# Optimization experiments

Hardware: AMD Instinct MI355X
Metric: run time of the kernel (lower is better)

Reference implementation:

```python
import jax, jax.numpy as jnp
import numpy as np

N_E = 1024
E_DIM = 512
LEGACY_CLUSTER = 0.2
LEGACY_ENERGY = 0.2


def setup_inputs() -> dict:
    key = jax.random.key(0)
    k1, k2 = jax.random.split(key)
    B, T = 64, 512
    key_soft = jax.random.normal(k1, (B, T, E_DIM), dtype=jnp.float32)
    zero_ts_mask = jnp.zeros((B,), dtype=bool)
    # nn.Embedding(1+n_e, e_dim) initialized uniform(-1/n_e, 1/n_e)
    emb_weight = jax.random.uniform(k2, (N_E + 1, E_DIM), dtype=jnp.float32,
                                    minval=-1.0 / N_E, maxval=1.0 / N_E)
    return {"key_soft": key_soft, "zero_ts_mask": zero_ts_mask, "emb_weight": emb_weight}


def _compute_indices(d3, zero_ts_mask, n_e):
    # d3: [B, T, n_e+1] squared distances (treated as constants: torch.no_grad)
    ind0 = jnp.clip(jnp.argmin(d3[:, 0, :], axis=1), 0, n_e - 1)
    ind0 = jnp.where(zero_ts_mask, 0, ind0)

    def step(ind, d_t):
        # d_t: [B, n_e+1]; neighbor-constrained argmin: stay at ind or move to ind+1
        d_here = jnp.take_along_axis(d_t, ind[:, None], axis=1)[:, 0]
        ind_next = jnp.clip(ind + 1, 0, n_e - 1)
        d_next = jnp.take_along_axis(d_t, ind_next[:, None], axis=1)[:, 0]
        new_ind = jnp.where(d_here <= d_next, ind, ind_next)
        return new_ind, new_ind

    d_rest = jnp.swapaxes(d3[:, 1:, :], 0, 1)  # [T-1, B, n_e+1] time-major
    _, inds_rest = jax.lax.scan(step, ind0, d_rest)
    return jnp.concatenate([ind0[:, None], jnp.swapaxes(inds_rest, 0, 1)], axis=1)  # [B, T]


def reference(key_soft, zero_ts_mask, emb_weight):
    sg = jax.lax.stop_gradient
    B, T, e_dim = key_soft.shape
    n_e = emb_weight.shape[0] - 1
    ksf = key_soft.reshape(-1, e_dim)  # [B*T, e_dim]
    # squared euclidean distances to all 1+n_e codes: [B*T, n_e+1]
    d = (jnp.sum(ksf ** 2, axis=1, keepdims=True)
         + jnp.sum(emb_weight ** 2, axis=1)
         - 2.0 * jnp.einsum('bd,nd->bn', ksf, emb_weight))
    min_indices = jnp.argmin(d, axis=1)  # [B*T]
    d3 = d.reshape(B, T, n_e + 1)
    encoding_indices = _compute_indices(sg(d3), zero_ts_mask, n_e)  # [B, T]

    key_hard_here = emb_weight[encoding_indices]        # [B, T, e_dim]
    key_hard_next = emb_weight[encoding_indices + 1]    # [B, T, e_dim]
    key_min = emb_weight[min_indices].reshape(B, T, e_dim)

    key_em_here = (jnp.sum((sg(key_soft) - key_hard_here) ** 2, axis=-1)
                   + jnp.sum((key_soft - sg(key_hard_here)) ** 2, axis=-1) * LEGACY_ENERGY)
    key_em_next = (jnp.sum((sg(key_soft) - key_hard_next) ** 2, axis=-1)
                   + jnp.sum((key_soft - sg(key_hard_next)) ** 2, axis=-1) * LEGACY_ENERGY)
    key_energy_mat = key_em_next - key_em_here  # [B, T]

    ind_change = (encoding_indices[:, 1:] - encoding_indices[:, :-1]).astype(bool)
    key_energy_change = (key_energy_mat[:, 1:] - key_energy_mat[:, :-1]) * jnp.where(ind_change, 0.0, 1.0)
    eps = 1e-06 / n_e
    loss_key_energy_descent = jnp.maximum(key_energy_change + eps, 0.0).mean()

    loss_min_indices = (jnp.sum((sg(key_soft) - key_min) ** 2, axis=-1)
                        + jnp.sum((key_soft - sg(key_min)) ** 2, axis=-1) * LEGACY_CLUSTER)
    reg_persist_mat = jnp.exp(-key_em_next)
    e_normal_mat = jnp.where(key_em_here > loss_min_indices - eps,
                             key_em_here - loss_min_indices + eps,
                             key_em_here) + reg_persist_mat
    e_abnormal_mat = key_em_next + jnp.exp(-key_em_here)

    key_hard = key_soft + sg(key_hard_here - key_soft)  # straight-through
    v = jnp.max(jnp.max(encoding_indices, axis=1) - jnp.min(encoding_indices, axis=1))
    return (key_hard, encoding_indices, v, loss_key_energy_descent,
            key_energy_mat, e_normal_mat, e_abnormal_mat)
```

## Files before the change

kernel.cpp:

```cpp
#include <hip/hip_runtime.h>
#include <math.h>

typedef unsigned char u8;
typedef unsigned short u16;
typedef unsigned int u32;
typedef __attribute__((ext_vector_type(8))) short bf16x8;
typedef __attribute__((ext_vector_type(4))) float f32x4;

#define O1 16777216
#define O2 16809984
#define O3 16809985
#define O4 16809986
#define O5 16842754
#define O6 16875522

#define W_COLSQ 0
#define W_MINV  4352
#define W_MINI  2101504
#define W_SF    4198656
#define W_SL    6426880
#define W_BITS  8524032
#define W_MIDX  12718336
#define W_ENC   12849408
#define W_V     12980480
#define W_EH    13000704
#define W_EL    14050304

__device__ __forceinline__ u32 cvt_pk(float lo, float hi) {
  u32 r;
  asm volatile("v_cvt_pk_bf16_f32 %0, %1, %2" : "=v"(r) : "v"(lo), "v"(hi));
  return r;
}
__device__ __forceinline__ float asf(u32 u) { return __uint_as_float(u); }

__device__ __forceinline__ void gload_lds16(const void* g, void* l) {
  __builtin_amdgcn_global_load_lds(
      (const __attribute__((address_space(1))) unsigned int*)g,
      (__attribute__((address_space(3))) unsigned int*)l, 16, 0, 0);
}

__global__ __launch_bounds__(256) void k0_colsq(const float* __restrict__ emb,
                                                float* __restrict__ colsq,
                                                u32* __restrict__ emb_hi,
                                                u32* __restrict__ emb_lo) {
  int w = threadIdx.x >> 6, lane = threadIdx.x & 63;
  int c = blockIdx.x * 4 + w;
  if (c >= 1025) return;
  const float4* e4 = (const float4*)(emb + (size_t)c * 512);
  float4 a = e4[lane * 2], b = e4[lane * 2 + 1];
  float p = a.x * a.x + a.y * a.y + a.z * a.z + a.w * a.w
          + b.x * b.x + b.y * b.y + b.z * b.z + b.w * b.w;
  #pragma unroll
  for (int off = 32; off; off >>= 1) p += __shfl_xor(p, off);
  if (lane == 0) colsq[c] = p;
  u32 h0 = cvt_pk(a.x, a.y), h1 = cvt_pk(a.z, a.w);
  u32 h2 = cvt_pk(b.x, b.y), h3 = cvt_pk(b.z, b.w);
  float l0 = a.x - asf(h0 << 16), l1 = a.y - asf(h0 & 0xFFFF0000u);
  float l2 = a.z - asf(h1 << 16), l3 = a.w - asf(h1 & 0xFFFF0000u);
  float l4 = b.x - asf(h2 << 16), l5 = b.y - asf(h2 & 0xFFFF0000u);
  float l6 = b.z - asf(h3 << 16), l7 = b.w - asf(h3 & 0xFFFF0000u);
  uint4 hv; hv.x = h0; hv.y = h1; hv.z = h2; hv.w = h3;
  uint4 lv; lv.x = cvt_pk(l0, l1); lv.y = cvt_pk(l2, l3);
  lv.z = cvt_pk(l4, l5); lv.w = cvt_pk(l6, l7);
  ((uint4*)emb_hi)[c * 64 + lane] = hv;
  ((uint4*)emb_lo)[c * 64 + lane] = lv;
}

__global__ __launch_bounds__(256) void k1_gemm(const float* __restrict__ ksf,
                                               const u32* __restrict__ emb_hi,
                                               const u32* __restrict__ emb_lo,
                                               const float* __restrict__ colsq,
                                               float* __restrict__ minv, int* __restrict__ mini,
                                               float* __restrict__ sF, float* __restrict__ sL,
                                               u8* __restrict__ bits) {
  __shared__ float smemf[8448];
  char* smc = (char*)smemf;
  const int tid = threadIdx.x, bid = blockIdx.x;
  const int g = bid >> 6;
  const int cbk = (bid >> 3) & 7;
  const int rb = g * 8 + (bid & 7);
  const int r0 = rb * 128, c0 = cbk * 128;
  const int lane = tid & 63, w = tid >> 6;
  const int wr = w >> 1, wc = w & 1;
  const int q = lane >> 4, li = lane & 15;

  int offS[4], baseA[4];
  #pragma unroll
  for (int i = 0; i < 4; i++) {
    int p = tid + (i << 8);
    int row = p >> 3, q8 = p & 7;
    offS[i] = row * 64 + ((q8 * 8) ^ (((row >> 1) & 3) << 4));
    baseA[i] = (r0 + row) * 128 + q8;
  }
  const int rowj0 = w * 32 + (lane >> 2), rowj1 = rowj0 + 16;
  const int qb = lane & 3;
  const int offB0 = (c0 + rowj0) * 1024 + ((qb ^ ((rowj0 >> 1) & 3)) << 4);
  const int offB1 = (c0 + rowj1) * 1024 + ((qb ^ ((rowj1 >> 1) & 3)) << 4);
  char* ldsB0 = smc + 16384 + w * 2048;
  char* ldsB1 = ldsB0 + 1024;
  const char* ebh = (const char*)emb_hi;
  const char* ebl = (const char*)emb_lo;

  int foA[4], foB[4];
  #pragma unroll
  for (int m = 0; m < 4; m++) {
    int row = wr * 64 + m * 16 + li;
    foA[m] = row * 64 + ((q * 16) ^ (((row >> 1) & 3) << 4));
    int col = wc * 64 + m * 16 + li;
    foB[m] = col * 64 + ((q * 16) ^ (((col >> 1) & 3) << 4));
  }

  f32x4 acc[4][4];
  #pragma unroll
  for (int m = 0; m < 4; m++)
    #pragma unroll
    for (int n = 0; n < 4; n++) acc[m][n] = (f32x4){0.f, 0.f, 0.f, 0.f};

  const float4* A4 = (const float4*)ksf;
  float4 ra[4];
  #pragma unroll
  for (int i = 0; i < 4; i++) ra[i] = A4[baseA[i]];

  for (int kt = 0; kt < 16; kt++) {
    __syncthreads();
    {
      int ko = kt * 64;
      gload_lds16(ebh + offB0 + ko, ldsB0);
      gload_lds16(ebh + offB1 + ko, ldsB1);
      gload_lds16(ebl + offB0 + ko, ldsB0 + 8192);
      gload_lds16(ebl + offB1 + ko, ldsB1 + 8192);
    }
    #pragma unroll
    for (int i = 0; i < 4; i++) {
      float4 v = ra[i];
      u32 w0 = cvt_pk(v.x, v.y), w1 = cvt_pk(v.z, v.w);
      float lx = v.x - asf(w0 << 16);
      float ly = v.y - asf(w0 & 0xFFFF0000u);
      float lz = v.z - asf(w1 << 16);
      float lw = v.w - asf(w1 & 0xFFFF0000u);
      u32 m0 = cvt_pk(lx, ly), m1 = cvt_pk(lz, lw);
      uint2 hv; hv.x = w0; hv.y = w1;
      uint2 lv; lv.x = m0; lv.y = m1;
      *(uint2*)(smc + offS[i]) = hv;
      *(uint2*)(smc + 8192 + offS[i]) = lv;
    }
    __syncthreads();
    if (kt < 15) {
      #pragma unroll
      for (int i = 0; i < 4; i++) ra[i] = A4[baseA[i] + (kt + 1) * 8];
    }
    bf16x8 fA[4], fB[4], fX[4];
    #pragma unroll
    for (int m = 0; m < 4; m++) fA[m] = *(const bf16x8*)(smc + foA[m]);
    #pragma unroll
    for (int n = 0; n < 4; n++) fB[n] = *(const bf16x8*)(smc + 16384 + foB[n]);
    #pragma unroll
    for (int m = 0; m < 4; m++)
      #pragma unroll
      for (int n = 0; n < 4; n++)
        acc[m][n] = __builtin_amdgcn_mfma_f32_16x16x32_bf16(fA[m], fB[n], acc[m][n], 0, 0, 0);
    #pragma unroll
    for (int n = 0; n < 4; n++) fX[n] = *(const bf16x8*)(smc + 24576 + foB[n]);
    #pragma unroll
    for (int m = 0; m < 4; m++)
      #pragma unroll
      for (int n = 0; n < 4; n++)
        acc[m][n] = __builtin_amdgcn_mfma_f32_16x16x32_bf16(fA[m], fX[n], acc[m][n], 0, 0, 0);
    #pragma unroll
    for (int m = 0; m < 4; m++) fA[m] = *(const bf16x8*)(smc + 8192 + foA[m]);
    #pragma unroll
    for (int m = 0; m < 4; m++)
      #pragma unroll
      for (int n = 0; n < 4; n++)
        acc[m][n] = __builtin_amdgcn_mfma_f32_16x16x32_bf16(fA[m], fB[n], acc[m][n], 0, 0, 0);
  }

  float cs4[4];
  #pragma unroll
  for (int n = 0; n < 4; n++) cs4[n] = colsq[c0 + wc * 64 + n * 16 + li];
  const int ct = tid & 15, rt = tid >> 4;
  for (int h = 0; h < 2; h++) {
    __syncthreads();
    if (wr == h) {
      #pragma unroll
      for (int m = 0; m < 4; m++) {
        int rl = m * 16 + q * 4;
        #pragma unroll
        for (int n = 0; n < 4; n++) {
          int cl = wc * 64 + n * 16 + li;
          #pragma unroll
          for (int r = 0; r < 4; r++)
            smemf[(rl + r) * 132 + cl] = fmaf(acc[m][n][r], -2.0f, cs4[n]);
        }
      }
    }
    __syncthreads();
    #pragma unroll
    for (int j = 0; j < 4; j++) {
      int rl = rt * 4 + j;
      int rowg = r0 + h * 64 + rl;
      const float* sp = &smemf[rl * 132 + ct * 8];
      float4 sa = *(const float4*)sp, sb = *(const float4*)(sp + 4);
      float s[8] = {sa.x, sa.y, sa.z, sa.w, sb.x, sb.y, sb.z, sb.w};
      float sn0 = __shfl_down(s[0], 1, 16);
      u32 bv = 0;
      #pragma unroll
      for (int i = 0; i < 7; i++) bv |= (s[i] <= s[i + 1]) ? (1u << i) : 0u;
      bv |= (s[7] <= sn0) ? 0x80u : 0u;
      bits[rowg * 128 + cbk * 16 + ct] = (u8)bv;
      int cbase = c0 + ct * 8;
      float mv = s[0]; int mi = cbase;
      #pragma unroll
      for (int i = 1; i < 8; i++) if (s[i] < mv) { mv = s[i]; mi = cbase + i; }
      #pragma unroll
      for (int d = 4; d >= 1; d >>= 1) {
        float ov = __shfl_xor(mv, d, 8);
        int oi = __shfl_xor(mi, d, 8);
        if (ov < mv || (ov == mv && oi < mi)) { mv = ov; mi = oi; }
      }
      int sb64 = cbk * 2 + (ct >> 3);
      if ((ct & 7) == 0) {
        minv[rowg * 16 + sb64] = mv;
        mini[rowg * 16 + sb64] = mi;
        sF[rowg * 17 + sb64] = s[0];
      }
      if ((ct & 7) == 7) sL[rowg * 16 + sb64] = s[7];
    }
  }
}

__global__ __launch_bounds__(256) void k1b_col1024(const float* __restrict__ ksf,
                                                   const float* __restrict__ emb,
                                                   const float* __restrict__ colsq,
                                                   float* __restrict__ sF) {
  int wid = threadIdx.x >> 6, lane = threadIdx.x & 63;
  int row = blockIdx.x * 4 + wid;
  const float4* ks4 = (const float4*)(ksf + (size_t)row * 512);
  const float4* e4 = (const float4*)(emb + (size_t)1024 * 512);
  float4 a = ks4[lane * 2], b = ks4[lane * 2 + 1];
  float4 ea = e4[lane * 2], eb = e4[lane * 2 + 1];
  float p = a.x * ea.x + a.y * ea.y + a.z * ea.z + a.w * ea.w
          + b.x * eb.x + b.y * eb.y + b.z * eb.z + b.w * eb.w;
  #pragma unroll
  for (int off = 32; off; off >>= 1) p += __shfl_xor(p, off);
  if (lane == 0) sF[row * 17 + 16] = fmaf(p, -2.0f, colsq[1024]);
}

__global__ __launch_bounds__(256) void k2_combine(const float* __restrict__ minv,
                                                  const int* __restrict__ mini,
                                                  const float* __restrict__ sF,
                                                  const float* __restrict__ sL,
                                                  u8* __restrict__ bits,
                                                  int* __restrict__ midx, int* __restrict__ vslot) {
  int row = blockIdx.x * 256 + threadIdx.x;
  if (blockIdx.x == 0 && threadIdx.x == 0) *vslot = 0;
  float bv = minv[row * 16];
  int bi = mini[row * 16];
  #pragma unroll
  for (int cb = 1; cb < 16; cb++) {
    float v = minv[row * 16 + cb];
    int ii = mini[row * 16 + cb];
    if (v < bv) { bv = v; bi = ii; }
  }
  float s1024 = sF[row * 17 + 16];
  if (s1024 < bv) { bv = s1024; bi = 1024; }
  midx[row] = bi;
  #pragma unroll
  for (int cb = 0; cb < 16; cb++) {
    float nb = (cb < 15) ? sF[row * 17 + cb + 1] : s1024;
    u8 bit = (sL[row * 16 + cb] <= nb) ? (u8)0x80 : (u8)0;
    int a = row * 128 + cb * 8 + 7;
    bits[a] = (u8)((bits[a] & 0x7F) | bit);
  }
}

__global__ __launch_bounds__(256) void k3_scan(const u8* __restrict__ bits,
                                               const int* __restrict__ midx,
                                               const u8* __restrict__ mask,
                                               int* __restrict__ enc, int* __restrict__ vslot) {
  __shared__ u32 bl[256 * 32];
  __shared__ int el[512];
  int b = blockIdx.x, tid = threadIdx.x;
  const u32* bw = (const u32*)bits;
  for (int phase = 0; phase < 2; phase++) {
    int t0 = 1 + phase * 256;
    int nt = phase ? 255 : 256;
    __syncthreads();
    for (int w = tid; w < nt * 32; w += 256)
      bl[w] = bw[(size_t)(b * 512 + t0) * 32 + w];
    __syncthreads();
    if (tid == 0) {
      int ind;
      if (phase == 0) {
        int mi = midx[b * 512];
        ind = mi < 1023 ? mi : 1023;
        if (mask[b]) ind = 0;
        el[0] = ind;
      } else ind = el[256];
      for (int tt = 0; tt < nt; tt++) {
        if (ind < 1023) {
          u32 w = bl[tt * 32 + (ind >> 5)];
          ind += 1 - (int)((w >> (ind & 31)) & 1u);
        }
        el[t0 + tt] = ind;
      }
    }
  }
  __syncthreads();
  for (int t = tid; t < 512; t += 256) enc[b * 512 + t] = el[t];
  if (tid == 0) atomicMax(vslot, el[511] - el[0]);
}

__global__ __launch_bounds__(256) void k4_energy(const float* __restrict__ ksf,
                                                 const float* __restrict__ emb,
                                                 const int* __restrict__ enc_a,
                                                 const int* __restrict__ midx,
                                                 float* __restrict__ out) {
  int wid = threadIdx.x >> 6, lane = threadIdx.x & 63;
  int row = blockIdx.x * 4 + wid;
  int eh = enc_a[row];
  int mi = midx[row];
  const float4* ks4 = (const float4*)(ksf + (size_t)row * 512);
  const float4* h4 = (const float4*)(emb + (size_t)eh * 512);
  const float4* n4 = (const float4*)(emb + (size_t)(eh + 1) * 512);
  const float4* m4 = (const float4*)(emb + (size_t)mi * 512);
  float ph = 0.f, pn = 0.f, pm = 0.f;
  float4 kh[2];
  #pragma unroll
  for (int u = 0; u < 2; u++) {
    float4 k = ks4[lane * 2 + u], h = h4[lane * 2 + u], n = n4[lane * 2 + u], m = m4[lane * 2 + u];
    float d;
    d = k.x - h.x; ph = fmaf(d, d, ph);
    d = k.y - h.y; ph = fmaf(d, d, ph);
    d = k.z - h.z; ph = fmaf(d, d, ph);
    d = k.w - h.w; ph = fmaf(d, d, ph);
    d = k.x - n.x; pn = fmaf(d, d, pn);
    d = k.y - n.y; pn = fmaf(d, d, pn);
    d = k.z - n.z; pn = fmaf(d, d, pn);
    d = k.w - n.w; pn = fmaf(d, d, pn);
    d = k.x - m.x; pm = fmaf(d, d, pm);
    d = k.y - m.y; pm = fmaf(d, d, pm);
    d = k.z - m.z; pm = fmaf(d, d, pm);
    d = k.w - m.w; pm = fmaf(d, d, pm);
    kh[u].x = k.x + (h.x - k.x);
    kh[u].y = k.y + (h.y - k.y);
    kh[u].z = k.z + (h.z - k.z);
    kh[u].w = k.w + (h.w - k.w);
  }
  #pragma unroll
  for (int off = 32; off; off >>= 1) {
    ph += __shfl_xor(ph, off);
    pn += __shfl_xor(pn, off);
    pm += __shfl_xor(pm, off);
  }
  float4* o0 = (float4*)out;
  o0[(size_t)row * 128 + lane * 2] = kh[0];
  o0[(size_t)row * 128 + lane * 2 + 1] = kh[1];
  if (lane == 0) {
    const float epsN = 9.765625e-10f;
    float kemh = ph + ph * 0.2f;
    float kemn = pn + pn * 0.2f;
    float lmin = pm + pm * 0.2f;
    float lminu = fminf(lmin, kemh);
    out[O1 + row] = (float)eh;
    out[O4 + row] = kemn - kemh;
    float env = (kemh > lminu - epsN) ? ((kemh - lminu) + epsN) : kemh;
    out[O5 + row] = env + expf(-kemn);
    out[O6 + row] = kemn + expf(-kemh);
  }
}

__global__ __launch_bounds__(1024) void k5_loss(const float* __restrict__ kem,
                                                const int* __restrict__ enc,
                                                const int* __restrict__ vslot,
                                                float* __restrict__ out) {
  __shared__ float red[1024];
  int tid = threadIdx.x;
  const float epsN = 9.765625e-10f;
  float p = 0.f;
  for (int i = tid; i < 64 * 511; i += 1024) {
    int b = i / 511, tt = i - b * 511;
    int row = b * 512 + tt + 1;
    float diff = kem[row] - kem[row - 1];
    if (enc[row] != enc[row - 1]) diff = 0.f;
    float v = diff + epsN;
    p += (v > 0.f) ? v : 0.f;
  }
  red[tid] = p;
  __syncthreads();
  for (int s = 512; s; s >>= 1) {
    if (tid < s) red[tid] += red[tid + s];
    __syncthreads();
  }
  if (tid == 0) {
    out[O3] = red[0] / 32704.0f;
    out[O2] = (float)(*vslot);
  }
}

extern "C" void kernel_launch(void* const* d_in, const int* in_sizes, int n_in,
                              void* d_out, int out_size, void* d_ws, size_t ws_size,
                              hipStream_t stream) {
  const float* ksf = (const float*)d_in[0];
  const u8* mask = (const u8*)d_in[1];
  const float* emb = (const float*)d_in[2];
  float* out = (float*)d_out;
  char* ws = (char*)d_ws;
  float* colsq = (float*)(ws + W_COLSQ);
  float* minv = (float*)(ws + W_MINV);
  int* mini = (int*)(ws + W_MINI);
  float* sF = (float*)(ws + W_SF);
  float* sL = (float*)(ws + W_SL);
  u8* bits = (u8*)(ws + W_BITS);
  int* midx = (int*)(ws + W_MIDX);
  int* enc = (int*)(ws + W_ENC);
  int* vslot = (int*)(ws + W_V);
  u32* emb_hi = (u32*)(ws + W_EH);
  u32* emb_lo = (u32*)(ws + W_EL);

  hipLaunchKernelGGL(k0_colsq, dim3(257), dim3(256), 0, stream, emb, colsq, emb_hi, emb_lo);
  hipLaunchKernelGGL(k1_gemm, dim3(2048), dim3(256), 0, stream, ksf, emb_hi, emb_lo, colsq,
                     minv, mini, sF, sL, bits);
  hipLaunchKernelGGL(k1b_col1024, dim3(8192), dim3(256), 0, stream, ksf, emb, colsq, sF);
  hipLaunchKernelGGL(k2_combine, dim3(128), dim3(256), 0, stream, minv, mini, sF, sL,
                     bits, midx, vslot);
  hipLaunchKernelGGL(k3_scan, dim3(64), dim3(256), 0, stream, bits, midx, mask, enc, vslot);
  hipLaunchKernelGGL(k4_energy, dim3(8192), dim3(256), 0, stream, ksf, emb, enc, midx, out);
  hipLaunchKernelGGL(k5_loss, dim3(1), dim3(1024), 0, stream, out + O4, enc, vslot, out);
}
```

Measured before the change: 228.0 us.

## Double-buffer GEMM LDS stages and vectorize sequential index scan across a wavefront

The distance GEMM now uses two LDS buffers, loading the next K-tile into one while MFMAs read the other, which halves the barriers per tile and raises wave priority around the MFMA phase. Separately, the serial per-batch neighbor scan, formerly run by a single thread, is restructured so 64 lanes gather transposed bit masks for 64 candidate positions and the walk proceeds via readlane, cutting LDS latency per step. Bounds clamps on indices are also added. The cost is double the shared memory, which lowers occupancy, plus more bit-gather work in the scan.

```diff
diff --git a/kernel.cpp b/kernel.cpp
--- a/kernel.cpp
+++ b/kernel.cpp
@@ -73,7 +73,7 @@
                                                float* __restrict__ minv, int* __restrict__ mini,
                                                float* __restrict__ sF, float* __restrict__ sL,
                                                u8* __restrict__ bits) {
-  __shared__ float smemf[8448];
+  __shared__ float smemf[16384];
   char* smc = (char*)smemf;
   const int tid = threadIdx.x, bid = blockIdx.x;
   const int g = bid >> 6;
@@ -96,8 +96,6 @@
   const int qb = lane & 3;
   const int offB0 = (c0 + rowj0) * 1024 + ((qb ^ ((rowj0 >> 1) & 3)) << 4);
   const int offB1 = (c0 + rowj1) * 1024 + ((qb ^ ((rowj1 >> 1) & 3)) << 4);
-  char* ldsB0 = smc + 16384 + w * 2048;
-  char* ldsB1 = ldsB0 + 1024;
   const char* ebh = (const char*)emb_hi;
   const char* ebl = (const char*)emb_lo;
 
@@ -118,18 +116,16 @@
 
   const float4* A4 = (const float4*)ksf;
   float4 ra[4];
-  #pragma unroll
-  for (int i = 0; i < 4; i++) ra[i] = A4[baseA[i]];
-
-  for (int kt = 0; kt < 16; kt++) {
-    __syncthreads();
-    {
-      int ko = kt * 64;
-      gload_lds16(ebh + offB0 + ko, ldsB0);
-      gload_lds16(ebh + offB1 + ko, ldsB1);
-      gload_lds16(ebl + offB0 + ko, ldsB0 + 8192);
-      gload_lds16(ebl + offB1 + ko, ldsB1 + 8192);
-    }
+
+  auto stageB = [&](int bb, int t1) {
+    int ko = t1 * 64;
+    char* d0 = smc + bb + 16384 + w * 2048;
+    gload_lds16(ebh + offB0 + ko, d0);
+    gload_lds16(ebh + offB1 + ko, d0 + 1024);
+    gload_lds16(ebl + offB0 + ko, d0 + 8192);
+    gload_lds16(ebl + offB1 + ko, d0 + 9216);
+  };
+  auto stageA = [&](int bb) {
     #pragma unroll
     for (int i = 0; i < 4; i++) {
       float4 v = ra[i];
@@ -141,38 +137,75 @@
       u32 m0 = cvt_pk(lx, ly), m1 = cvt_pk(lz, lw);
       uint2 hv; hv.x = w0; hv.y = w1;
       uint2 lv; lv.x = m0; lv.y = m1;
-      *(uint2*)(smc + offS[i]) = hv;
-      *(uint2*)(smc + 8192 + offS[i]) = lv;
-    }
-    __syncthreads();
-    if (kt < 15) {
-      #pragma unroll
-      for (int i = 0; i < 4; i++) ra[i] = A4[baseA[i] + (kt + 1) * 8];
-    }
+      *(uint2*)(smc + bb + offS[i]) = hv;
+      *(uint2*)(smc + bb + 8192 + offS[i]) = lv;
+    }
+  };
+  auto mfma_phase = [&](int bb) {
     bf16x8 fA[4], fB[4], fX[4];
     #pragma unroll
-    for (int m = 0; m < 4; m++) fA[m] = *(const bf16x8*)(smc + foA[m]);
-    #pragma unroll
-    for (int n = 0; n < 4; n++) fB[n] = *(const bf16x8*)(smc + 16384 + foB[n]);
+    for (int m = 0; m < 4; m++) fA[m] = *(const bf16x8*)(smc + bb + foA[m]);
+    #pragma unroll
+    for (int n = 0; n < 4; n++) fB[n] = *(const bf16x8*)(smc + bb + 16384 + foB[n]);
     #pragma unroll
     for (int m = 0; m < 4; m++)
       #pragma unroll
       for (int n = 0; n < 4; n++)
         acc[m][n] = __builtin_amdgcn_mfma_f32_16x16x32_bf16(fA[m], fB[n], acc[m][n], 0, 0, 0);
     #pragma unroll
-    for (int n = 0; n < 4; n++) fX[n] = *(const bf16x8*)(smc + 24576 + foB[n]);
+    for (int n = 0; n < 4; n++) fX[n] = *(const bf16x8*)(smc + bb + 24576 + foB[n]);
     #pragma unroll
     for (int m = 0; m < 4; m++)
       #pragma unroll
       for (int n = 0; n < 4; n++)
         acc[m][n] = __builtin_amdgcn_mfma_f32_16x16x32_bf16(fA[m], fX[n], acc[m][n], 0, 0, 0);
     #pragma unroll
-    for (int m = 0; m < 4; m++) fA[m] = *(const bf16x8*)(smc + 8192 + foA[m]);
+    for (int m = 0; m < 4; m++) fA[m] = *(const bf16x8*)(smc + bb + 8192 + foA[m]);
     #pragma unroll
     for (int m = 0; m < 4; m++)
       #pragma unroll
       for (int n = 0; n < 4; n++)
         acc[m][n] = __builtin_amdgcn_mfma_f32_16x16x32_bf16(fA[m], fB[n], acc[m][n], 0, 0, 0);
+  };
+
+  #pragma unroll
+  for (int i = 0; i < 4; i++) ra[i] = A4[baseA[i]];
+  stageB(0, 0);
+  stageA(0);
+  #pragma unroll
+  for (int i = 0; i < 4; i++) ra[i] = A4[baseA[i] + 8];
+  __syncthreads();
+
+  #pragma unroll 1
+  for (int tp = 0; tp < 8; tp++) {
+    int t = tp * 2;
+    {
+      stageB(32768, t + 1);
+      stageA(32768);
+      if (t < 14) {
+        #pragma unroll
+        for (int i = 0; i < 4; i++) ra[i] = A4[baseA[i] + (t + 2) * 8];
+      }
+      __builtin_amdgcn_s_setprio(1);
+      mfma_phase(0);
+      __builtin_amdgcn_s_setprio(0);
+      __syncthreads();
+    }
+    {
+      int t1 = t + 1;
+      if (t1 < 15) {
+        stageB(0, t1 + 1);
+        stageA(0);
+        if (t1 < 14) {
+          #pragma unroll
+          for (int i = 0; i < 4; i++) ra[i] = A4[baseA[i] + (t1 + 2) * 8];
+        }
+      }
+      __builtin_amdgcn_s_setprio(1);
+      mfma_phase(32768);
+      __builtin_amdgcn_s_setprio(0);
+      __syncthreads();
+    }
   }
 
   float cs4[4];
@@ -280,29 +313,54 @@
                                                int* __restrict__ enc, int* __restrict__ vslot) {
   __shared__ u32 bl[256 * 32];
   __shared__ int el[512];
-  int b = blockIdx.x, tid = threadIdx.x;
+  int b = blockIdx.x, tid = threadIdx.x, lane = tid & 63;
   const u32* bw = (const u32*)bits;
   for (int phase = 0; phase < 2; phase++) {
     int t0 = 1 + phase * 256;
     int nt = phase ? 255 : 256;
     __syncthreads();
-    for (int w = tid; w < nt * 32; w += 256)
-      bl[w] = bw[(size_t)(b * 512 + t0) * 32 + w];
+    for (int ww = tid; ww < nt * 32; ww += 256)
+      bl[ww] = bw[(size_t)(b * 512 + t0) * 32 + ww];
     __syncthreads();
-    if (tid == 0) {
+    if (tid < 64) {
       int ind;
       if (phase == 0) {
         int mi = midx[b * 512];
         ind = mi < 1023 ? mi : 1023;
+        if (ind < 0) ind = 0;
         if (mask[b]) ind = 0;
-        el[0] = ind;
-      } else ind = el[256];
-      for (int tt = 0; tt < nt; tt++) {
-        if (ind < 1023) {
-          u32 w = bl[tt * 32 + (ind >> 5)];
-          ind += 1 - (int)((w >> (ind & 31)) & 1u);
+        if (lane == 0) el[0] = ind;
+      } else {
+        ind = el[256];
+      }
+      int done = 0;
+      while (done < nt) {
+        int W = nt - done; if (W > 64) W = 64;
+        int i0 = ind;
+        int p = i0 + lane;
+        u32 mlo = 0xFFFFFFFFu, mhi = 0xFFFFFFFFu;
+        if (p < 1023) {
+          int base = done * 32 + (p >> 5);
+          int sh = p & 31;
+          mlo = 0; mhi = 0;
+          #pragma unroll
+          for (int s = 0; s < 32; s++)
+            mlo |= ((bl[base + s * 32] >> sh) & 1u) << s;
+          #pragma unroll
+          for (int s = 0; s < 32; s++)
+            mhi |= ((bl[base + (s + 32) * 32] >> sh) & 1u) << s;
         }
-        el[t0 + tt] = ind;
+        int rel = 0, myel = 0;
+        #pragma unroll
+        for (int s = 0; s < 64; s++) {
+          u32 wv = (s < 32) ? __builtin_amdgcn_readlane(mlo, rel)
+                            : __builtin_amdgcn_readlane(mhi, rel);
+          rel += 1 - (int)((wv >> (s & 31)) & 1u);
+          if (lane == s) myel = i0 + rel;
+        }
+        if (lane < W) el[t0 + done + lane] = myel;
+        ind = (int)__builtin_amdgcn_readlane((u32)myel, (u32)(W - 1));
+        done += W;
       }
     }
   }
@@ -320,6 +378,8 @@
   int row = blockIdx.x * 4 + wid;
   int eh = enc_a[row];
   int mi = midx[row];
+  eh = (eh < 0) ? 0 : (eh > 1023 ? 1023 : eh);
+  mi = (mi < 0) ? 0 : (mi > 1024 ? 1024 : mi);
   const float4* ks4 = (const float4*)(ksf + (size_t)row * 512);
   const float4* h4 = (const float4*)(emb + (size_t)eh * 512);
   const float4* n4 = (const float4*)(emb + (size_t)(eh + 1) * 512);
```

New measurement: 202.9 us. -11.0%, faster.
